# Kernel tuning notes

Hardware: AMD Instinct MI355X
Metric: run time of the kernel (lower is better)

Reference implementation:

```python
import jax, jax.numpy as jnp
import numpy as np


def setup_inputs() -> dict:
    key = jax.random.key(0)
    k1, k2, k3 = jax.random.split(key, 3)
    N, D, E = 16384, 4096, 64
    x = jax.random.normal(k1, (N, D), dtype=jnp.float32)
    W = jax.random.normal(k2, (E, D), dtype=jnp.float32) * (1.0 / np.sqrt(D))
    b = jax.random.normal(k3, (E,), dtype=jnp.float32) * 0.01
    return {"x": x, "W": W, "b": b, "top_k": 2}


def reference(x, W, b, top_k):
    # logits: [N, E]
    logits = jnp.einsum('nd,ed->ne', x, W) + b
    top_vals, top_idx = jax.lax.top_k(logits, top_k)          # [N, k]
    top_probs = jax.nn.softmax(top_vals, axis=-1)             # softmax over the k selected logits
    N = logits.shape[0]
    rows = jnp.arange(N)[:, None]                             # [N, 1]
    gates = jnp.zeros_like(logits).at[rows, top_idx].set(top_probs)  # sparse gate tensor [N, E]
    return gates, top_idx
```

## Files before the change

kernel.cpp:

```cpp
#include <hip/hip_runtime.h>
#include <math.h>

constexpr int D_DIM = 4096;
constexpr int E_DIM = 64;
constexpr int BM    = 64;
constexpr int BK    = 64;
constexpr int NTHREADS = 256;
constexpr int LDX = BM + 4;
constexpr int LDW = E_DIM + 4;
constexpr int LDL = E_DIM + 1;

__global__ __launch_bounds__(NTHREADS, 4) void gemm_partial_kernel(
    const float* __restrict__ x, const float* __restrict__ W,
    float* __restrict__ partials, int ksplit)
{
    __shared__ float smem[BM * LDX + BK * LDW];
    float* Xs = smem;
    float* Ws = smem + BM * LDX;

    const int tid  = threadIdx.x;
    const int tn   = tid & 15;
    const int tm   = tid >> 4;
    const int bx   = blockIdx.x;
    const int tile = bx / ksplit;
    const int split= bx % ksplit;
    const int row0 = tile * BM;
    const int dk   = D_DIM / ksplit;
    const int koff = split * dk;
    const int ktloc= dk / BK;

    const int sr  = tid >> 4;
    const int sc4 = tid & 15;
    const int we  = tid & 63;
    const int wc  = tid >> 6;

    float acc[4][4] = {};

    const float* xblk  = x + (size_t)row0 * D_DIM + koff;
    const float* wbase = W + koff;

    float4 xr[4], wr[4];
    auto load_tile = [&](int t) {
#pragma unroll
        for (int p = 0; p < 4; ++p)
            xr[p] = *(const float4*)(xblk + t * BK + (size_t)(p * 16 + sr) * D_DIM + sc4 * 4);
#pragma unroll
        for (int q = 0; q < 4; ++q)
            wr[q] = *(const float4*)(wbase + t * BK + (size_t)we * D_DIM + wc * 16 + q * 4);
    };
    auto store_tile = [&]() {
#pragma unroll
        for (int p = 0; p < 4; ++p)
            *(float4*)&Xs[(p * 16 + sr) * LDX + sc4 * 4] = xr[p];
#pragma unroll
        for (int q = 0; q < 4; ++q) {
            const int k = wc * 16 + q * 4;
            Ws[(k + 0) * LDW + we] = wr[q].x;
            Ws[(k + 1) * LDW + we] = wr[q].y;
            Ws[(k + 2) * LDW + we] = wr[q].z;
            Ws[(k + 3) * LDW + we] = wr[q].w;
        }
    };

    load_tile(0);
    store_tile();
    __syncthreads();

    for (int t = 0; t < ktloc; ++t) {
        if (t + 1 < ktloc) load_tile(t + 1);

#pragma unroll 4
        for (int kg = 0; kg < BK / 4; ++kg) {
            float4 wb0 = *(const float4*)&Ws[(kg * 4 + 0) * LDW + tn * 4];
            float4 wb1 = *(const float4*)&Ws[(kg * 4 + 1) * LDW + tn * 4];
            float4 wb2 = *(const float4*)&Ws[(kg * 4 + 2) * LDW + tn * 4];
            float4 wb3 = *(const float4*)&Ws[(kg * 4 + 3) * LDW + tn * 4];
#pragma unroll
            for (int i = 0; i < 4; ++i) {
                const float4 xa = *(const float4*)&Xs[(tm * 4 + i) * LDX + kg * 4];
                acc[i][0] += xa.x * wb0.x; acc[i][1] += xa.x * wb0.y;
                acc[i][2] += xa.x * wb0.z; acc[i][3] += xa.x * wb0.w;
                acc[i][0] += xa.y * wb1.x; acc[i][1] += xa.y * wb1.y;
                acc[i][2] += xa.y * wb1.z; acc[i][3] += xa.y * wb1.w;
                acc[i][0] += xa.z * wb2.x; acc[i][1] += xa.z * wb2.y;
                acc[i][2] += xa.z * wb2.z; acc[i][3] += xa.z * wb2.w;
                acc[i][0] += xa.w * wb3.x; acc[i][1] += xa.w * wb3.y;
                acc[i][2] += xa.w * wb3.z; acc[i][3] += xa.w * wb3.w;
            }
        }
        __syncthreads();
        if (t + 1 < ktloc) store_tile();
        __syncthreads();
    }

    float* my = partials + (size_t)bx * (BM * E_DIM);
#pragma unroll
    for (int i = 0; i < 4; ++i)
        *(float4*)(my + (tm * 4 + i) * E_DIM + tn * 4) =
            make_float4(acc[i][0], acc[i][1], acc[i][2], acc[i][3]);
}

__global__ __launch_bounds__(NTHREADS) void topk_finish_kernel(
    const float* __restrict__ partials, const float* __restrict__ b,
    float* __restrict__ out, int ksplit, int N)
{
    __shared__ float smem[BM * LDL + 256];
    float* Ls  = smem;
    float* aux = smem + BM * LDL;

    const int tid  = threadIdx.x;
    const int tile = blockIdx.x;
    const int row0 = tile * BM;
    const float* base = partials + (size_t)tile * ksplit * (BM * E_DIM);

#pragma unroll
    for (int p = 0; p < 4; ++p) {
        const int f4 = p * 256 + tid;
        const int r  = f4 >> 4;
        const int c4 = f4 & 15;
        float4 s = *(const float4*)(base + (size_t)f4 * 4);
        for (int sp = 1; sp < ksplit; ++sp) {
            const float4 t4 = *(const float4*)(base + (size_t)sp * (BM * E_DIM) + (size_t)f4 * 4);
            s.x += t4.x; s.y += t4.y; s.z += t4.z; s.w += t4.w;
        }
        const float4 bb = ((const float4*)b)[c4];
        Ls[r * LDL + c4 * 4 + 0] = s.x + bb.x;
        Ls[r * LDL + c4 * 4 + 1] = s.y + bb.y;
        Ls[r * LDL + c4 * 4 + 2] = s.z + bb.z;
        Ls[r * LDL + c4 * 4 + 3] = s.w + bb.w;
    }
    __syncthreads();

    if (tid < BM) {
        const float* lr = &Ls[tid * LDL];
        float v1 = -INFINITY, v2 = -INFINITY;
        int i1 = 0, i2 = 0;
        for (int e = 0; e < E_DIM; ++e) {
            const float v = lr[e];
            if (v > v1)      { v2 = v1; i2 = i1; v1 = v; i1 = e; }
            else if (v > v2) { v2 = v;  i2 = e; }
        }
        const float ex = expf(v2 - v1);
        const float dn = 1.0f + ex;
        aux[tid]       = (float)i1;
        aux[64 + tid]  = (float)i2;
        aux[128 + tid] = 1.0f / dn;
        aux[192 + tid] = ex / dn;
        const size_t basei = (size_t)N * E_DIM + (size_t)(row0 + tid) * 2;
        out[basei]     = (float)i1;
        out[basei + 1] = (float)i2;
    }
    __syncthreads();

#pragma unroll
    for (int p = 0; p < 4; ++p) {
        const int f4 = p * 256 + tid;
        const int r  = f4 >> 4;
        const int c4 = f4 & 15;
        const int i1 = (int)aux[r];
        const int i2 = (int)aux[64 + r];
        const float p1 = aux[128 + r];
        const float p2 = aux[192 + r];
        const int e = c4 * 4;
        float4 g;
        g.x = (e + 0 == i1) ? p1 : (e + 0 == i2) ? p2 : 0.0f;
        g.y = (e + 1 == i1) ? p1 : (e + 1 == i2) ? p2 : 0.0f;
        g.z = (e + 2 == i1) ? p1 : (e + 2 == i2) ? p2 : 0.0f;
        g.w = (e + 3 == i1) ? p1 : (e + 3 == i2) ? p2 : 0.0f;
        *(float4*)(out + (size_t)(row0 + r) * E_DIM + e) = g;
    }
}

extern "C" void kernel_launch(void* const* d_in, const int* in_sizes, int n_in,
                              void* d_out, int out_size, void* d_ws, size_t ws_size,
                              hipStream_t stream) {
    const float* x = (const float*)d_in[0];
    const float* W = (const float*)d_in[1];
    const float* b = (const float*)d_in[2];
    float* out = (float*)d_out;
    const int N = in_sizes[0] / D_DIM;
    const int ntiles = N / BM;

    const size_t pbytes = (size_t)BM * E_DIM * sizeof(float);
    int ksplit = 1;
    if      (ws_size >= (size_t)ntiles * 4 * pbytes) ksplit = 4;
    else if (ws_size >= (size_t)ntiles * 2 * pbytes) ksplit = 2;

    float* partials = (float*)d_ws;

    hipLaunchKernelGGL(gemm_partial_kernel, dim3(ntiles * ksplit), dim3(NTHREADS),
                       0, stream, x, W, partials, ksplit);
    hipLaunchKernelGGL(topk_finish_kernel, dim3(ntiles), dim3(NTHREADS),
                       0, stream, partials, b, out, ksplit, N);
}
```

Measured before the change: 464.5 us.

## Replace FP32 SIMT GEMM with split-FP16 MFMA and fuse top-k epilogue

Swaps the scalar FP32 FMA GEMM for MFMA 16x16x32 f16 instructions. Accuracy is kept by splitting both x and W into scaled hi/lo f16 halves and issuing three MFMAs per tile. W is pre-packed into hi/lo f16 buffers by a small kernel, and the split-K partials round trip is removed by doing the top-k and softmax epilogue inside the GEMM kernel. This trades extra conversion work and triple MFMA issue for far higher matrix throughput, but there is a risk that approximate logits flip top-k ties.

```diff
diff --git a/kernel.cpp b/kernel.cpp
--- a/kernel.cpp
+++ b/kernel.cpp
@@ -1,64 +1,102 @@
 #include <hip/hip_runtime.h>
 #include <math.h>
+
+typedef _Float16 f16;
+typedef _Float16 f16x8 __attribute__((ext_vector_type(8)));
+typedef _Float16 f16x4 __attribute__((ext_vector_type(4)));
+typedef float    f32x4 __attribute__((ext_vector_type(4)));
 
 constexpr int D_DIM = 4096;
 constexpr int E_DIM = 64;
 constexpr int BM    = 64;
 constexpr int BK    = 64;
-constexpr int NTHREADS = 256;
-constexpr int LDX = BM + 4;
-constexpr int LDW = E_DIM + 4;
-constexpr int LDL = E_DIM + 1;
-
-__global__ __launch_bounds__(NTHREADS, 4) void gemm_partial_kernel(
-    const float* __restrict__ x, const float* __restrict__ W,
-    float* __restrict__ partials, int ksplit)
+constexpr int NT    = 256;
+constexpr int LDT   = BK + 8;
+constexpr int LDL   = E_DIM + 1;
+
+constexpr float XSCALE  = 8.0f;
+constexpr float WSCALE  = 256.0f;
+constexpr float UNSCALE = 1.0f / 2048.0f;
+
+__global__ __launch_bounds__(NT) void pack_w(const float* __restrict__ W,
+                                             f16* __restrict__ whi,
+                                             f16* __restrict__ wlo) {
+    const int i = (blockIdx.x * NT + threadIdx.x) * 4;
+    const float4 w = *(const float4*)(W + i);
+    const float v[4] = {w.x * WSCALE, w.y * WSCALE, w.z * WSCALE, w.w * WSCALE};
+    f16x4 hv, lv;
+#pragma unroll
+    for (int j = 0; j < 4; ++j) {
+        const f16 h = (f16)v[j];
+        hv[j] = h;
+        lv[j] = (f16)(v[j] - (float)h);
+    }
+    *(f16x4*)(whi + i) = hv;
+    *(f16x4*)(wlo + i) = lv;
+}
+
+__global__ __launch_bounds__(NT) void gate_kernel(
+    const float* __restrict__ x, const f16* __restrict__ whi,
+    const f16* __restrict__ wlo, const float* __restrict__ b,
+    float* __restrict__ out, int N)
 {
-    __shared__ float smem[BM * LDX + BK * LDW];
-    float* Xs = smem;
-    float* Ws = smem + BM * LDX;
+    __shared__ alignas(16) f16 sm[4 * BM * LDT];
+    f16* Xh = sm;
+    f16* Xl = sm + BM * LDT;
+    f16* Wh = sm + 2 * BM * LDT;
+    f16* Wl = sm + 3 * BM * LDT;
 
     const int tid  = threadIdx.x;
-    const int tn   = tid & 15;
-    const int tm   = tid >> 4;
-    const int bx   = blockIdx.x;
-    const int tile = bx / ksplit;
-    const int split= bx % ksplit;
-    const int row0 = tile * BM;
-    const int dk   = D_DIM / ksplit;
-    const int koff = split * dk;
-    const int ktloc= dk / BK;
-
-    const int sr  = tid >> 4;
-    const int sc4 = tid & 15;
-    const int we  = tid & 63;
-    const int wc  = tid >> 6;
-
-    float acc[4][4] = {};
-
-    const float* xblk  = x + (size_t)row0 * D_DIM + koff;
-    const float* wbase = W + koff;
-
-    float4 xr[4], wr[4];
+    const int row0 = blockIdx.x * BM;
+
+    const int ks = tid & 7;
+    const int r8 = tid >> 3;
+
+    const int lane = tid & 63;
+    const int wv   = tid >> 6;
+    const int r0   = wv * 16;
+    const int m    = lane & 15;
+    const int quad = lane >> 4;
+
+    f32x4 acc[4] = {{0,0,0,0},{0,0,0,0},{0,0,0,0},{0,0,0,0}};
+
+    float4 xr[2][2];
+    f16x8 whr[2], wlr[2];
+
+    const float* xblk = x + (size_t)row0 * D_DIM;
+
     auto load_tile = [&](int t) {
-#pragma unroll
-        for (int p = 0; p < 4; ++p)
-            xr[p] = *(const float4*)(xblk + t * BK + (size_t)(p * 16 + sr) * D_DIM + sc4 * 4);
-#pragma unroll
-        for (int q = 0; q < 4; ++q)
-            wr[q] = *(const float4*)(wbase + t * BK + (size_t)we * D_DIM + wc * 16 + q * 4);
+        const int k0 = t * BK;
+#pragma unroll
+        for (int p = 0; p < 2; ++p) {
+            const int r = p * 32 + r8;
+            const float* xp = xblk + (size_t)r * D_DIM + k0 + ks * 8;
+            xr[p][0] = ((const float4*)xp)[0];
+            xr[p][1] = ((const float4*)xp)[1];
+            const size_t wo = (size_t)r * D_DIM + k0 + ks * 8;
+            whr[p] = *(const f16x8*)(whi + wo);
+            wlr[p] = *(const f16x8*)(wlo + wo);
+        }
     };
     auto store_tile = [&]() {
 #pragma unroll
-        for (int p = 0; p < 4; ++p)
-            *(float4*)&Xs[(p * 16 + sr) * LDX + sc4 * 4] = xr[p];
-#pragma unroll
-        for (int q = 0; q < 4; ++q) {
-            const int k = wc * 16 + q * 4;
-            Ws[(k + 0) * LDW + we] = wr[q].x;
-            Ws[(k + 1) * LDW + we] = wr[q].y;
-            Ws[(k + 2) * LDW + we] = wr[q].z;
-            Ws[(k + 3) * LDW + we] = wr[q].w;
+        for (int p = 0; p < 2; ++p) {
+            const int r = p * 32 + r8;
+            const float v[8] = {xr[p][0].x * XSCALE, xr[p][0].y * XSCALE,
+                                xr[p][0].z * XSCALE, xr[p][0].w * XSCALE,
+                                xr[p][1].x * XSCALE, xr[p][1].y * XSCALE,
+                                xr[p][1].z * XSCALE, xr[p][1].w * XSCALE};
+            f16x8 hv, lv;
+#pragma unroll
+            for (int j = 0; j < 8; ++j) {
+                const f16 h = (f16)v[j];
+                hv[j] = h;
+                lv[j] = (f16)(v[j] - (float)h);
+            }
+            *(f16x8*)&Xh[r * LDT + ks * 8] = hv;
+            *(f16x8*)&Xl[r * LDT + ks * 8] = lv;
+            *(f16x8*)&Wh[r * LDT + ks * 8] = whr[p];
+            *(f16x8*)&Wl[r * LDT + ks * 8] = wlr[p];
         }
     };
 
@@ -66,68 +104,41 @@
     store_tile();
     __syncthreads();
 
-    for (int t = 0; t < ktloc; ++t) {
-        if (t + 1 < ktloc) load_tile(t + 1);
-
-#pragma unroll 4
-        for (int kg = 0; kg < BK / 4; ++kg) {
-            float4 wb0 = *(const float4*)&Ws[(kg * 4 + 0) * LDW + tn * 4];
-            float4 wb1 = *(const float4*)&Ws[(kg * 4 + 1) * LDW + tn * 4];
-            float4 wb2 = *(const float4*)&Ws[(kg * 4 + 2) * LDW + tn * 4];
-            float4 wb3 = *(const float4*)&Ws[(kg * 4 + 3) * LDW + tn * 4];
-#pragma unroll
-            for (int i = 0; i < 4; ++i) {
-                const float4 xa = *(const float4*)&Xs[(tm * 4 + i) * LDX + kg * 4];
-                acc[i][0] += xa.x * wb0.x; acc[i][1] += xa.x * wb0.y;
-                acc[i][2] += xa.x * wb0.z; acc[i][3] += xa.x * wb0.w;
-                acc[i][0] += xa.y * wb1.x; acc[i][1] += xa.y * wb1.y;
-                acc[i][2] += xa.y * wb1.z; acc[i][3] += xa.y * wb1.w;
-                acc[i][0] += xa.z * wb2.x; acc[i][1] += xa.z * wb2.y;
-                acc[i][2] += xa.z * wb2.z; acc[i][3] += xa.z * wb2.w;
-                acc[i][0] += xa.w * wb3.x; acc[i][1] += xa.w * wb3.y;
-                acc[i][2] += xa.w * wb3.z; acc[i][3] += xa.w * wb3.w;
+    constexpr int KT = D_DIM / BK;
+    for (int t = 0; t < KT; ++t) {
+        if (t + 1 < KT) load_tile(t + 1);
+
+#pragma unroll
+        for (int kk = 0; kk < 2; ++kk) {
+            const int ko = kk * 32 + quad * 8;
+            const f16x8 ah = *(const f16x8*)&Xh[(r0 + m) * LDT + ko];
+            const f16x8 al = *(const f16x8*)&Xl[(r0 + m) * LDT + ko];
+#pragma unroll
+            for (int ct = 0; ct < 4; ++ct) {
+                const f16x8 bh = *(const f16x8*)&Wh[(ct * 16 + m) * LDT + ko];
+                const f16x8 bl = *(const f16x8*)&Wl[(ct * 16 + m) * LDT + ko];
+                acc[ct] = __builtin_amdgcn_mfma_f32_16x16x32_f16(ah, bh, acc[ct], 0, 0, 0);
+                acc[ct] = __builtin_amdgcn_mfma_f32_16x16x32_f16(ah, bl, acc[ct], 0, 0, 0);
+                acc[ct] = __builtin_amdgcn_mfma_f32_16x16x32_f16(al, bh, acc[ct], 0, 0, 0);
             }
         }
         __syncthreads();
-        if (t + 1 < ktloc) store_tile();
+        if (t + 1 < KT) store_tile();
         __syncthreads();
     }
 
-    float* my = partials + (size_t)bx * (BM * E_DIM);
-#pragma unroll
-    for (int i = 0; i < 4; ++i)
-        *(float4*)(my + (tm * 4 + i) * E_DIM + tn * 4) =
-            make_float4(acc[i][0], acc[i][1], acc[i][2], acc[i][3]);
-}
-
-__global__ __launch_bounds__(NTHREADS) void topk_finish_kernel(
-    const float* __restrict__ partials, const float* __restrict__ b,
-    float* __restrict__ out, int ksplit, int N)
-{
-    __shared__ float smem[BM * LDL + 256];
-    float* Ls  = smem;
-    float* aux = smem + BM * LDL;
-
-    const int tid  = threadIdx.x;
-    const int tile = blockIdx.x;
-    const int row0 = tile * BM;
-    const float* base = partials + (size_t)tile * ksplit * (BM * E_DIM);
-
-#pragma unroll
-    for (int p = 0; p < 4; ++p) {
-        const int f4 = p * 256 + tid;
-        const int r  = f4 >> 4;
-        const int c4 = f4 & 15;
-        float4 s = *(const float4*)(base + (size_t)f4 * 4);
-        for (int sp = 1; sp < ksplit; ++sp) {
-            const float4 t4 = *(const float4*)(base + (size_t)sp * (BM * E_DIM) + (size_t)f4 * 4);
-            s.x += t4.x; s.y += t4.y; s.z += t4.z; s.w += t4.w;
-        }
-        const float4 bb = ((const float4*)b)[c4];
-        Ls[r * LDL + c4 * 4 + 0] = s.x + bb.x;
-        Ls[r * LDL + c4 * 4 + 1] = s.y + bb.y;
-        Ls[r * LDL + c4 * 4 + 2] = s.z + bb.z;
-        Ls[r * LDL + c4 * 4 + 3] = s.w + bb.w;
+    float* Ls  = (float*)sm;
+    float* aux = Ls + BM * LDL;
+
+#pragma unroll
+    for (int ct = 0; ct < 4; ++ct) {
+        const int col = ct * 16 + m;
+        const float bb = b[col];
+#pragma unroll
+        for (int reg = 0; reg < 4; ++reg) {
+            const int row = r0 + quad * 4 + reg;
+            Ls[row * LDL + col] = acc[ct][reg] * UNSCALE + bb;
+        }
     }
     __syncthreads();
 
@@ -179,17 +190,12 @@
     const float* b = (const float*)d_in[2];
     float* out = (float*)d_out;
     const int N = in_sizes[0] / D_DIM;
-    const int ntiles = N / BM;
-
-    const size_t pbytes = (size_t)BM * E_DIM * sizeof(float);
-    int ksplit = 1;
-    if      (ws_size >= (size_t)ntiles * 4 * pbytes) ksplit = 4;
-    else if (ws_size >= (size_t)ntiles * 2 * pbytes) ksplit = 2;
-
-    float* partials = (float*)d_ws;
-
-    hipLaunchKernelGGL(gemm_partial_kernel, dim3(ntiles * ksplit), dim3(NTHREADS),
-                       0, stream, x, W, partials, ksplit);
-    hipLaunchKernelGGL(topk_finish_kernel, dim3(ntiles), dim3(NTHREADS),
-                       0, stream, partials, b, out, ksplit, N);
+
+    f16* whi = (f16*)d_ws;
+    f16* wlo = whi + (size_t)E_DIM * D_DIM;
+
+    hipLaunchKernelGGL(pack_w, dim3((E_DIM * D_DIM) / (NT * 4)), dim3(NT),
+                       0, stream, W, whi, wlo);
+    hipLaunchKernelGGL(gate_kernel, dim3(N / BM), dim3(NT),
+                       0, stream, x, whi, wlo, b, out, N);
 }
```

New measurement: 405.1 us. -12.8%, faster.
